# Kernel tuning notes

Hardware: AMD Instinct MI355X
Metric: run time of the kernel (lower is better)

## Reference

```python
import jax, jax.numpy as jnp
import numpy as np

B = 131072          # batch of fermion configurations
S = 256             # sys_size
NUP = 16            # num_fillings[0]
NDOWN = 16          # num_fillings[1]


def _random_occupancy(rng, b, s, nfill):
    # exactly `nfill` ones per row, uniformly random positions
    r = rng.random((b, s))
    perm_rank = np.argsort(r, axis=1).argsort(axis=1)  # a random permutation per row
    return (perm_rank < nfill).astype(np.float32)


def setup_inputs() -> dict:
    rng = np.random.default_rng(0)
    cfg_up = _random_occupancy(rng, B, S, NUP)
    cfg_down = _random_occupancy(rng, B, S, NDOWN)
    config_fermion = jnp.asarray(np.concatenate([cfg_up, cfg_down], axis=1))  # (B, 2S)
    key = jax.random.key(0)
    k1, k2 = jax.random.split(key)
    states_up = jax.random.normal(k1, (S, NUP), dtype=jnp.float32)
    states_down = jax.random.normal(k2, (S, NDOWN), dtype=jnp.float32)
    return {"config_fermion": config_fermion, "states_up": states_up, "states_down": states_down}


def reference(config_fermion, states_up, states_down):
    s = states_up.shape[0]
    nup = states_up.shape[1]
    ndown = states_down.shape[1]
    cfg_up = config_fermion[:, :s]      # (B, S) of {0,1}
    cfg_down = config_fermion[:, s:]
    # indices of occupied sites, ascending (torch.nonzero order); top_k breaks
    # ties by lowest index, then sort ascending
    idx_up = jnp.sort(jax.lax.top_k(cfg_up, nup)[1], axis=1)        # (B, Nup)
    idx_down = jnp.sort(jax.lax.top_k(cfg_down, ndown)[1], axis=1)  # (B, Ndown)
    mats_up = states_up[idx_up]         # (B, Nup, Nup) gather of orbital rows
    mats_down = states_down[idx_down]   # (B, Ndown, Ndown)
    det_up = jnp.linalg.det(mats_up)
    det_down = jnp.linalg.det(mats_down)
    return det_up * det_down
```

## Files before the change

### kernel.cpp

```cpp
#include <hip/hip_runtime.h>

static __device__ __forceinline__ unsigned umax2(unsigned a, unsigned b) { return a > b ? a : b; }

static __device__ __forceinline__ float qb(float v, int sel) {
    int i = __float_as_int(v), r;
    switch (sel) {
        case 0:  r = __builtin_amdgcn_update_dpp(0, i, 0x00, 0xF, 0xF, true); break;
        case 1:  r = __builtin_amdgcn_update_dpp(0, i, 0x55, 0xF, 0xF, true); break;
        case 2:  r = __builtin_amdgcn_update_dpp(0, i, 0xAA, 0xF, 0xF, true); break;
        default: r = __builtin_amdgcn_update_dpp(0, i, 0xFF, 0xF, 0xF, true); break;
    }
    return __int_as_float(r);
}

static __device__ __forceinline__ int mbcnt64(unsigned long long m, int acc) {
    acc = __builtin_amdgcn_mbcnt_lo((unsigned)m, acc);
    acc = __builtin_amdgcn_mbcnt_hi((unsigned)(m >> 32), acc);
    return acc;
}

__global__ __launch_bounds__(256) void slater_det_main(
    const float* __restrict__ cfg,
    const float* __restrict__ sup,
    const float* __restrict__ sdn,
    float* __restrict__ out,
    unsigned* __restrict__ ws_count,
    unsigned* __restrict__ ws_rec,
    unsigned cap)
{
    __shared__ __align__(16) int idx_lds[4][16][16];

    const int tid  = threadIdx.x;
    const int wave = tid >> 6;
    const int lane = tid & 63;
    const int wb0  = (blockIdx.x * 4 + wave) * 8;

    float4 c[16];
#pragma unroll
    for (int d = 0; d < 16; ++d) {
        const float* p = cfg + (size_t)wb0 * 512 + (size_t)d * 256 + (size_t)lane * 4;
        c[d] = *(const float4*)p;
    }
#pragma unroll
    for (int d = 0; d < 16; ++d) {
        float4 v = c[d];
        bool n0 = v.x != 0.f, n1 = v.y != 0.f, n2 = v.z != 0.f, n3 = v.w != 0.f;
        unsigned long long b0 = __ballot(n0);
        unsigned long long b1 = __ballot(n1);
        unsigned long long b2 = __ballot(n2);
        unsigned long long b3 = __ballot(n3);
        int base = mbcnt64(b3, mbcnt64(b2, mbcnt64(b1, mbcnt64(b0, 0))));
        int pos = lane * 4;
        int r = base;
        if (n0 && r < 16) idx_lds[wave][d][r] = pos;
        r += n0;
        if (n1 && r < 16) idx_lds[wave][d][r] = pos + 1;
        r += n1;
        if (n2 && r < 16) idx_lds[wave][d][r] = pos + 2;
        r += n2;
        if (n3 && r < 16) idx_lds[wave][d][r] = pos + 3;
    }
    asm volatile("s_waitcnt lgkmcnt(0)" ::: "memory");
    __builtin_amdgcn_sched_barrier(0);

    const int g = lane >> 2;
    const int q = lane & 3;
    const int4 ri = *(const int4*)&idx_lds[wave][g][q * 4];
    const float* tab = (g & 1) ? sdn : sup;
    const int rid[4] = {ri.x, ri.y, ri.z, ri.w};

    float rr[4][16];
#pragma unroll
    for (int j = 0; j < 4; ++j) {
        const float* p = tab + (size_t)rid[j] * 16;
        float4 a = *(const float4*)(p + 0);
        float4 b = *(const float4*)(p + 4);
        float4 e = *(const float4*)(p + 8);
        float4 f = *(const float4*)(p + 12);
        rr[j][0]=a.x;  rr[j][1]=a.y;  rr[j][2]=a.z;  rr[j][3]=a.w;
        rr[j][4]=b.x;  rr[j][5]=b.y;  rr[j][6]=b.z;  rr[j][7]=b.w;
        rr[j][8]=e.x;  rr[j][9]=e.y;  rr[j][10]=e.z; rr[j][11]=e.w;
        rr[j][12]=f.x; rr[j][13]=f.y; rr[j][14]=f.z; rr[j][15]=f.w;
    }

    float det = 1.f;
    bool bad = false;
#pragma unroll
    for (int k = 0; k < 16; ++k) {
        const int sel = k >> 2;
        const int jp  = k & 3;
        float piv = qb(rr[jp][k], sel);
        det *= piv;
        bad = bad || (fabsf(piv) < 1e-4f);
        float inv = __builtin_amdgcn_rcpf(piv);
        float f0 = rr[0][k] * inv;
        float f1 = rr[1][k] * inv;
        float f2 = rr[2][k] * inv;
        float f3 = rr[3][k] * inv;
#pragma unroll
        for (int cc = k + 1; cc < 16; ++cc) {
            float pcc = qb(rr[jp][cc], sel);
            rr[0][cc] = __builtin_fmaf(-f0, pcc, rr[0][cc]);
            rr[1][cc] = __builtin_fmaf(-f1, pcc, rr[1][cc]);
            rr[2][cc] = __builtin_fmaf(-f2, pcc, rr[2][cc]);
            rr[3][cc] = __builtin_fmaf(-f3, pcc, rr[3][cc]);
        }
    }

    int badflag = bad ? 1 : 0;
    int partnerbad = __shfl_xor(badflag, 4);
    if ((badflag | partnerbad) && (lane & 7) == 0) {
        unsigned slot = atomicAdd(ws_count, 1u);
        if (slot < cap) {
            unsigned* rec = ws_rec + slot * 12;
            rec[0] = (unsigned)(wb0 + (lane >> 3));
            const int gU = lane >> 2;
#pragma unroll
            for (int t = 0; t < 4; ++t) {
                const int* iu = &idx_lds[wave][gU][t * 4];
                const int* id = &idx_lds[wave][gU | 1][t * 4];
                rec[1 + t] = (unsigned)iu[0] | ((unsigned)iu[1] << 8)
                           | ((unsigned)iu[2] << 16) | ((unsigned)iu[3] << 24);
                rec[5 + t] = (unsigned)id[0] | ((unsigned)id[1] << 8)
                           | ((unsigned)id[2] << 16) | ((unsigned)id[3] << 24);
            }
        }
    }

    float prod = det * __shfl_xor(det, 4);
    if ((lane & 7) == 0) out[wb0 + (lane >> 3)] = prod;
}

__global__ __launch_bounds__(256) void slater_det_cleanup(
    const float* __restrict__ sup,
    const float* __restrict__ sdn,
    float* __restrict__ out,
    const unsigned* __restrict__ ws_count,
    const unsigned* __restrict__ ws_rec,
    unsigned cap)
{
    unsigned n = *ws_count;
    if (n > cap) n = cap;
    const int tid  = blockIdx.x * 256 + threadIdx.x;
    const int unit = tid >> 3;
    const int nunits = (int)(gridDim.x * 256) >> 3;
    const int l8   = threadIdx.x & 7;
    const int wl   = threadIdx.x & 63;
    const int q    = wl & 3;
    const int gbase = wl & ~3;

    for (unsigned item = unit; item < n; item += nunits) {
        const unsigned* rec = ws_rec + item * 12;
        const unsigned batch = rec[0];
        const int half = l8 >> 2;
        const unsigned pk = rec[1 + half * 4 + q];
        const int rid[4] = { (int)(pk & 255u), (int)((pk >> 8) & 255u),
                             (int)((pk >> 16) & 255u), (int)(pk >> 24) };
        const float* tab = half ? sdn : sup;

        float rr[4][16];
#pragma unroll
        for (int j = 0; j < 4; ++j) {
            const float* p = tab + (size_t)rid[j] * 16;
            float4 a = *(const float4*)(p + 0);
            float4 b = *(const float4*)(p + 4);
            float4 e = *(const float4*)(p + 8);
            float4 f = *(const float4*)(p + 12);
            rr[j][0]=a.x;  rr[j][1]=a.y;  rr[j][2]=a.z;  rr[j][3]=a.w;
            rr[j][4]=b.x;  rr[j][5]=b.y;  rr[j][6]=b.z;  rr[j][7]=b.w;
            rr[j][8]=e.x;  rr[j][9]=e.y;  rr[j][10]=e.z; rr[j][11]=e.w;
            rr[j][12]=f.x; rr[j][13]=f.y; rr[j][14]=f.z; rr[j][15]=f.w;
        }

        unsigned am = 0xFu;
        float fdet = 1.f;
        int flips = 0;
#pragma unroll
        for (int k = 0; k < 16; ++k) {
            unsigned a0 = (__float_as_uint(rr[0][k]) & 0x7FFFFFF0u) | (unsigned)(q*4+0);
            unsigned a1 = (__float_as_uint(rr[1][k]) & 0x7FFFFFF0u) | (unsigned)(q*4+1);
            unsigned a2 = (__float_as_uint(rr[2][k]) & 0x7FFFFFF0u) | (unsigned)(q*4+2);
            unsigned a3 = (__float_as_uint(rr[3][k]) & 0x7FFFFFF0u) | (unsigned)(q*4+3);
            unsigned key0 = (am & 1u) ? a0 : (unsigned)(q*4+0);
            unsigned key1 = (am & 2u) ? a1 : (unsigned)(q*4+1);
            unsigned key2 = (am & 4u) ? a2 : (unsigned)(q*4+2);
            unsigned key3 = (am & 8u) ? a3 : (unsigned)(q*4+3);
            unsigned kloc = umax2(umax2(key0, key1), umax2(key2, key3));
            int jloc = (int)(kloc & 3u);
            float crow[16];
#pragma unroll
            for (int cc = k; cc < 16; ++cc) {
                float t01 = (jloc & 1) ? rr[1][cc] : rr[0][cc];
                float t23 = (jloc & 1) ? rr[3][cc] : rr[2][cc];
                crow[cc] = (jloc & 2) ? t23 : t01;
            }
            unsigned ko = kloc;
            ko = umax2(ko, (unsigned)__shfl_xor((int)ko, 1));
            ko = umax2(ko, (unsigned)__shfl_xor((int)ko, 2));
            int p   = (int)(ko & 15u);
            int src = gbase | (p >> 2);
            float prow[16];
#pragma unroll
            for (int cc = k; cc < 16; ++cc) prow[cc] = __shfl(crow[cc], src);
            float piv = prow[k];
            fdet *= piv;
            int t = p - q * 4;
            unsigned mlt = (t <= 0) ? 0u : ((t >= 4) ? 0xFu : ((1u << t) - 1u));
            int cnt = __popc(am & mlt);
            cnt += __shfl_xor(cnt, 1);
            cnt += __shfl_xor(cnt, 2);
            flips += cnt;
            if (q == (p >> 2)) am &= ~(1u << (p & 3));
            float inv = 1.0f / piv;
            float f0 = rr[0][k] * inv;
            float f1 = rr[1][k] * inv;
            float f2 = rr[2][k] * inv;
            float f3 = rr[3][k] * inv;
#pragma unroll
            for (int cc = k + 1; cc < 16; ++cc) {
                rr[0][cc] = __builtin_fmaf(-f0, prow[cc], rr[0][cc]);
                rr[1][cc] = __builtin_fmaf(-f1, prow[cc], rr[1][cc]);
                rr[2][cc] = __builtin_fmaf(-f2, prow[cc], rr[2][cc]);
                rr[3][cc] = __builtin_fmaf(-f3, prow[cc], rr[3][cc]);
            }
        }
        float det = (flips & 1) ? -fdet : fdet;
        float prod = det * __shfl_xor(det, 4);
        if (l8 == 0) out[batch] = prod;
    }
}

extern "C" void kernel_launch(void* const* d_in, const int* in_sizes, int n_in,
                              void* d_out, int out_size, void* d_ws, size_t ws_size,
                              hipStream_t stream) {
    const float* cfg = (const float*)d_in[0];
    const float* sup = (const float*)d_in[1];
    const float* sdn = (const float*)d_in[2];
    float* outp = (float*)d_out;
    unsigned* ws_count = (unsigned*)d_ws;
    unsigned* ws_rec   = (unsigned*)d_ws + 4;
    unsigned cap = (unsigned)((ws_size - 16) / 48);
    const int B = in_sizes[0] / 512;
    const int blocks = B / 32;

    hipMemsetAsync(d_ws, 0, 16, stream);
    slater_det_main<<<blocks, 256, 0, stream>>>(cfg, sup, sdn, outp,
                                                ws_count, ws_rec, cap);
    slater_det_cleanup<<<16, 256, 0, stream>>>(sup, sdn, outp,
                                               ws_count, ws_rec, cap);
}
```

Baseline: 69.49 us.

## Make main kernel persistent and prefetch next chunk during elimination

The main kernel becomes a persistent grid of 1024 blocks, with each wave looping over chunks of 8 configurations in a grid-stride pattern. The first half of the next chunk's configuration rows is prefetched into registers while the current determinant elimination runs, so global loads overlap with compute. The bad-pivot check now uses a running minimum, and the r<16 guards on the index stores are dropped, which assumes exactly 16 occupied sites per half. The risks are the extra live registers from the prefetch buffer lowering occupancy, and LDS index reuse across iterations with no barrier beyond the lgkmcnt wait.

```diff
diff --git a/kernel.cpp b/kernel.cpp
--- a/kernel.cpp
+++ b/kernel.cpp
@@ -26,109 +26,146 @@
     float* __restrict__ out,
     unsigned* __restrict__ ws_count,
     unsigned* __restrict__ ws_rec,
-    unsigned cap)
+    unsigned cap,
+    int nchunks)
 {
     __shared__ __align__(16) int idx_lds[4][16][16];
 
     const int tid  = threadIdx.x;
     const int wave = tid >> 6;
     const int lane = tid & 63;
-    const int wb0  = (blockIdx.x * 4 + wave) * 8;
-
-    float4 c[16];
-#pragma unroll
-    for (int d = 0; d < 16; ++d) {
-        const float* p = cfg + (size_t)wb0 * 512 + (size_t)d * 256 + (size_t)lane * 4;
-        c[d] = *(const float4*)p;
-    }
-#pragma unroll
-    for (int d = 0; d < 16; ++d) {
-        float4 v = c[d];
-        bool n0 = v.x != 0.f, n1 = v.y != 0.f, n2 = v.z != 0.f, n3 = v.w != 0.f;
-        unsigned long long b0 = __ballot(n0);
-        unsigned long long b1 = __ballot(n1);
-        unsigned long long b2 = __ballot(n2);
-        unsigned long long b3 = __ballot(n3);
-        int base = mbcnt64(b3, mbcnt64(b2, mbcnt64(b1, mbcnt64(b0, 0))));
-        int pos = lane * 4;
-        int r = base;
-        if (n0 && r < 16) idx_lds[wave][d][r] = pos;
-        r += n0;
-        if (n1 && r < 16) idx_lds[wave][d][r] = pos + 1;
-        r += n1;
-        if (n2 && r < 16) idx_lds[wave][d][r] = pos + 2;
-        r += n2;
-        if (n3 && r < 16) idx_lds[wave][d][r] = pos + 3;
-    }
-    asm volatile("s_waitcnt lgkmcnt(0)" ::: "memory");
-    __builtin_amdgcn_sched_barrier(0);
+    const int wgid = blockIdx.x * 4 + wave;
+    const int nw   = gridDim.x * 4;
 
     const int g = lane >> 2;
     const int q = lane & 3;
-    const int4 ri = *(const int4*)&idx_lds[wave][g][q * 4];
     const float* tab = (g & 1) ? sdn : sup;
-    const int rid[4] = {ri.x, ri.y, ri.z, ri.w};
-
-    float rr[4][16];
-#pragma unroll
-    for (int j = 0; j < 4; ++j) {
-        const float* p = tab + (size_t)rid[j] * 16;
-        float4 a = *(const float4*)(p + 0);
-        float4 b = *(const float4*)(p + 4);
-        float4 e = *(const float4*)(p + 8);
-        float4 f = *(const float4*)(p + 12);
-        rr[j][0]=a.x;  rr[j][1]=a.y;  rr[j][2]=a.z;  rr[j][3]=a.w;
-        rr[j][4]=b.x;  rr[j][5]=b.y;  rr[j][6]=b.z;  rr[j][7]=b.w;
-        rr[j][8]=e.x;  rr[j][9]=e.y;  rr[j][10]=e.z; rr[j][11]=e.w;
-        rr[j][12]=f.x; rr[j][13]=f.y; rr[j][14]=f.z; rr[j][15]=f.w;
+
+    float4 c[8];
+    int cur = wgid;
+    if (cur >= nchunks) return;
+
+#pragma unroll
+    for (int d = 0; d < 8; ++d)
+        c[d] = *(const float4*)(cfg + (size_t)cur * 4096 + (size_t)d * 256 + (size_t)lane * 4);
+
+    while (cur < nchunks) {
+        const int nxt = cur + nw;
+
+#pragma unroll
+        for (int d = 0; d < 8; ++d) {
+            float4 v = c[d];
+            bool n0 = v.x != 0.f, n1 = v.y != 0.f, n2 = v.z != 0.f, n3 = v.w != 0.f;
+            unsigned long long b0 = __ballot(n0);
+            unsigned long long b1 = __ballot(n1);
+            unsigned long long b2 = __ballot(n2);
+            unsigned long long b3 = __ballot(n3);
+            int r = mbcnt64(b3, mbcnt64(b2, mbcnt64(b1, mbcnt64(b0, 0))));
+            int pos = lane * 4;
+            if (n0) idx_lds[wave][d][r] = pos;
+            r += n0;
+            if (n1) idx_lds[wave][d][r] = pos + 1;
+            r += n1;
+            if (n2) idx_lds[wave][d][r] = pos + 2;
+            r += n2;
+            if (n3) idx_lds[wave][d][r] = pos + 3;
+        }
+#pragma unroll
+        for (int d = 0; d < 8; ++d)
+            c[d] = *(const float4*)(cfg + (size_t)cur * 4096 + (size_t)(d + 8) * 256 + (size_t)lane * 4);
+#pragma unroll
+        for (int d = 0; d < 8; ++d) {
+            float4 v = c[d];
+            bool n0 = v.x != 0.f, n1 = v.y != 0.f, n2 = v.z != 0.f, n3 = v.w != 0.f;
+            unsigned long long b0 = __ballot(n0);
+            unsigned long long b1 = __ballot(n1);
+            unsigned long long b2 = __ballot(n2);
+            unsigned long long b3 = __ballot(n3);
+            int r = mbcnt64(b3, mbcnt64(b2, mbcnt64(b1, mbcnt64(b0, 0))));
+            int pos = lane * 4;
+            if (n0) idx_lds[wave][d + 8][r] = pos;
+            r += n0;
+            if (n1) idx_lds[wave][d + 8][r] = pos + 1;
+            r += n1;
+            if (n2) idx_lds[wave][d + 8][r] = pos + 2;
+            r += n2;
+            if (n3) idx_lds[wave][d + 8][r] = pos + 3;
+        }
+        asm volatile("s_waitcnt lgkmcnt(0)" ::: "memory");
+
+        const int4 ri = *(const int4*)&idx_lds[wave][g][q * 4];
+        const int rid[4] = {ri.x, ri.y, ri.z, ri.w};
+
+        float rr[4][16];
+#pragma unroll
+        for (int j = 0; j < 4; ++j) {
+            const float* p = tab + (size_t)rid[j] * 16;
+            float4 a = *(const float4*)(p + 0);
+            float4 b = *(const float4*)(p + 4);
+            float4 e = *(const float4*)(p + 8);
+            float4 f = *(const float4*)(p + 12);
+            rr[j][0]=a.x;  rr[j][1]=a.y;  rr[j][2]=a.z;  rr[j][3]=a.w;
+            rr[j][4]=b.x;  rr[j][5]=b.y;  rr[j][6]=b.z;  rr[j][7]=b.w;
+            rr[j][8]=e.x;  rr[j][9]=e.y;  rr[j][10]=e.z; rr[j][11]=e.w;
+            rr[j][12]=f.x; rr[j][13]=f.y; rr[j][14]=f.z; rr[j][15]=f.w;
+        }
+
+        if (nxt < nchunks) {
+#pragma unroll
+            for (int d = 0; d < 8; ++d)
+                c[d] = *(const float4*)(cfg + (size_t)nxt * 4096 + (size_t)d * 256 + (size_t)lane * 4);
+        }
+
+        float det = 1.f;
+        float minpiv = 1.f;
+#pragma unroll
+        for (int k = 0; k < 16; ++k) {
+            const int sel = k >> 2;
+            const int jp  = k & 3;
+            float piv = qb(rr[jp][k], sel);
+            det *= piv;
+            minpiv = fminf(minpiv, fabsf(piv));
+            float inv = __builtin_amdgcn_rcpf(piv);
+            float f0 = rr[0][k] * inv;
+            float f1 = rr[1][k] * inv;
+            float f2 = rr[2][k] * inv;
+            float f3 = rr[3][k] * inv;
+#pragma unroll
+            for (int cc = k + 1; cc < 16; ++cc) {
+                float pcc = qb(rr[jp][cc], sel);
+                rr[0][cc] = __builtin_fmaf(-f0, pcc, rr[0][cc]);
+                rr[1][cc] = __builtin_fmaf(-f1, pcc, rr[1][cc]);
+                rr[2][cc] = __builtin_fmaf(-f2, pcc, rr[2][cc]);
+                rr[3][cc] = __builtin_fmaf(-f3, pcc, rr[3][cc]);
+            }
+        }
+        bool bad = minpiv < 1e-4f;
+
+        int badflag = bad ? 1 : 0;
+        int partnerbad = __shfl_xor(badflag, 4);
+        if ((badflag | partnerbad) && (lane & 7) == 0) {
+            unsigned slot = atomicAdd(ws_count, 1u);
+            if (slot < cap) {
+                unsigned* rec = ws_rec + slot * 12;
+                rec[0] = (unsigned)(cur * 8 + (lane >> 3));
+                const int gU = lane >> 2;
+#pragma unroll
+                for (int t = 0; t < 4; ++t) {
+                    const int* iu = &idx_lds[wave][gU][t * 4];
+                    const int* id = &idx_lds[wave][gU | 1][t * 4];
+                    rec[1 + t] = (unsigned)iu[0] | ((unsigned)iu[1] << 8)
+                               | ((unsigned)iu[2] << 16) | ((unsigned)iu[3] << 24);
+                    rec[5 + t] = (unsigned)id[0] | ((unsigned)id[1] << 8)
+                               | ((unsigned)id[2] << 16) | ((unsigned)id[3] << 24);
+                }
+            }
+        }
+
+        float prod = det * __shfl_xor(det, 4);
+        if ((lane & 7) == 0) out[cur * 8 + (lane >> 3)] = prod;
+
+        cur = nxt;
     }
-
-    float det = 1.f;
-    bool bad = false;
-#pragma unroll
-    for (int k = 0; k < 16; ++k) {
-        const int sel = k >> 2;
-        const int jp  = k & 3;
-        float piv = qb(rr[jp][k], sel);
-        det *= piv;
-        bad = bad || (fabsf(piv) < 1e-4f);
-        float inv = __builtin_amdgcn_rcpf(piv);
-        float f0 = rr[0][k] * inv;
-        float f1 = rr[1][k] * inv;
-        float f2 = rr[2][k] * inv;
-        float f3 = rr[3][k] * inv;
-#pragma unroll
-        for (int cc = k + 1; cc < 16; ++cc) {
-            float pcc = qb(rr[jp][cc], sel);
-            rr[0][cc] = __builtin_fmaf(-f0, pcc, rr[0][cc]);
-            rr[1][cc] = __builtin_fmaf(-f1, pcc, rr[1][cc]);
-            rr[2][cc] = __builtin_fmaf(-f2, pcc, rr[2][cc]);
-            rr[3][cc] = __builtin_fmaf(-f3, pcc, rr[3][cc]);
-        }
-    }
-
-    int badflag = bad ? 1 : 0;
-    int partnerbad = __shfl_xor(badflag, 4);
-    if ((badflag | partnerbad) && (lane & 7) == 0) {
-        unsigned slot = atomicAdd(ws_count, 1u);
-        if (slot < cap) {
-            unsigned* rec = ws_rec + slot * 12;
-            rec[0] = (unsigned)(wb0 + (lane >> 3));
-            const int gU = lane >> 2;
-#pragma unroll
-            for (int t = 0; t < 4; ++t) {
-                const int* iu = &idx_lds[wave][gU][t * 4];
-                const int* id = &idx_lds[wave][gU | 1][t * 4];
-                rec[1 + t] = (unsigned)iu[0] | ((unsigned)iu[1] << 8)
-                           | ((unsigned)iu[2] << 16) | ((unsigned)iu[3] << 24);
-                rec[5 + t] = (unsigned)id[0] | ((unsigned)id[1] << 8)
-                           | ((unsigned)id[2] << 16) | ((unsigned)id[3] << 24);
-            }
-        }
-    }
-
-    float prod = det * __shfl_xor(det, 4);
-    if ((lane & 7) == 0) out[wb0 + (lane >> 3)] = prod;
 }
 
 __global__ __launch_bounds__(256) void slater_det_cleanup(
@@ -241,11 +278,11 @@
     unsigned* ws_rec   = (unsigned*)d_ws + 4;
     unsigned cap = (unsigned)((ws_size - 16) / 48);
     const int B = in_sizes[0] / 512;
-    const int blocks = B / 32;
+    const int nchunks = B / 8;
 
     hipMemsetAsync(d_ws, 0, 16, stream);
-    slater_det_main<<<blocks, 256, 0, stream>>>(cfg, sup, sdn, outp,
-                                                ws_count, ws_rec, cap);
+    slater_det_main<<<1024, 256, 0, stream>>>(cfg, sup, sdn, outp,
+                                              ws_count, ws_rec, cap, nchunks);
     slater_det_cleanup<<<16, 256, 0, stream>>>(sup, sdn, outp,
                                                ws_count, ws_rec, cap);
 }
```

Result: faster. 67.52 us (-2.8%).

## Add warp-specialized producer/consumer pipeline streaming configs into an LDS ring

Applied to the files above, without the earlier changes.

Rewrites the main kernel as a producer/consumer design. One wave streams configuration rows into a 16-slot LDS ring using async global_load_lds with a prefetch depth of 12. Three consumer waves spin on per-slot ready and free flags, extract occupied indices and compute the determinants. Each block now handles 128 configs instead of 32, so there are fewer blocks. The aim is to overlap the memory-bound config loads with compute, at the cost of dedicating a quarter of the waves to loading plus spin-wait synchronisation overhead and lower occupancy from the larger LDS footprint.

```diff
diff --git a/kernel.cpp b/kernel.cpp
--- a/kernel.cpp
+++ b/kernel.cpp
@@ -1,4 +1,8 @@
 #include <hip/hip_runtime.h>
+
+#define NBPB 128
+#define RS   16
+#define PD   12
 
 static __device__ __forceinline__ unsigned umax2(unsigned a, unsigned b) { return a > b ? a : b; }
 
@@ -19,7 +23,13 @@
     return acc;
 }
 
-__global__ __launch_bounds__(256) void slater_det_main(
+static __device__ __forceinline__ void gload16(const float* g, void* l) {
+    __builtin_amdgcn_global_load_lds(
+        (const __attribute__((address_space(1))) unsigned*)g,
+        (__attribute__((address_space(3))) unsigned*)l, 16, 0, 0);
+}
+
+__global__ __launch_bounds__(256) void slater_pc(
     const float* __restrict__ cfg,
     const float* __restrict__ sup,
     const float* __restrict__ sdn,
@@ -28,107 +38,139 @@
     unsigned* __restrict__ ws_rec,
     unsigned cap)
 {
-    __shared__ __align__(16) int idx_lds[4][16][16];
+    __shared__ __align__(16) unsigned char ring[RS][2048];
+    __shared__ int idx_scr[3][8][2][16];
+    __shared__ int readyf[RS];
+    __shared__ int freef[RS];
 
     const int tid  = threadIdx.x;
     const int wave = tid >> 6;
     const int lane = tid & 63;
-    const int wb0  = (blockIdx.x * 4 + wave) * 8;
-
-    float4 c[16];
-#pragma unroll
-    for (int d = 0; d < 16; ++d) {
-        const float* p = cfg + (size_t)wb0 * 512 + (size_t)d * 256 + (size_t)lane * 4;
-        c[d] = *(const float4*)p;
+    const int b0   = blockIdx.x * NBPB;
+
+    if (tid < RS) { readyf[tid] = 0; freef[tid] = 0; }
+    __syncthreads();
+
+    volatile int* vready = readyf;
+    volatile int* vfree  = freef;
+
+    if (wave == 3) {
+        for (int s = 0; s < PD; ++s) {
+            const float* g = cfg + (size_t)(b0 + s) * 512 + (size_t)lane * 4;
+            gload16(g,       &ring[s][0]);
+            gload16(g + 256, &ring[s][1024]);
+        }
+        for (int s = 0; s < NBPB; ++s) {
+            const int t = s + PD;
+            if (t < NBPB) {
+                const int k = t & (RS - 1), gen = t >> 4;
+                while (vfree[k] != gen) __builtin_amdgcn_s_sleep(2);
+                const float* g = cfg + (size_t)(b0 + t) * 512 + (size_t)lane * 4;
+                gload16(g,       &ring[k][0]);
+                gload16(g + 256, &ring[k][1024]);
+                asm volatile("s_waitcnt vmcnt(24)" ::: "memory");
+            } else {
+                asm volatile("s_waitcnt vmcnt(0)" ::: "memory");
+            }
+            if (lane == 0) vready[s & (RS - 1)] = s + 1;
+        }
+    } else {
+        const int g = lane >> 2;
+        const int q = lane & 3;
+        const float* tab = (g & 1) ? sdn : sup;
+
+        for (int grp = wave; grp < NBPB / 8; grp += 3) {
+            for (int j = 0; j < 8; ++j) {
+                const int b = grp * 8 + j, k = b & (RS - 1);
+                while (vready[k] != b + 1) __builtin_amdgcn_s_sleep(2);
+                __builtin_amdgcn_sched_barrier(0);
+#pragma unroll
+                for (int h = 0; h < 2; ++h) {
+                    float4 v = *(const float4*)&ring[k][h * 1024 + lane * 16];
+                    bool n0 = v.x != 0.f, n1 = v.y != 0.f, n2 = v.z != 0.f, n3 = v.w != 0.f;
+                    unsigned long long m0 = __ballot(n0);
+                    unsigned long long m1 = __ballot(n1);
+                    unsigned long long m2 = __ballot(n2);
+                    unsigned long long m3 = __ballot(n3);
+                    int r = mbcnt64(m3, mbcnt64(m2, mbcnt64(m1, mbcnt64(m0, 0))));
+                    int pos = lane * 4;
+                    if (n0) idx_scr[wave][j][h][r] = pos;
+                    r += n0;
+                    if (n1) idx_scr[wave][j][h][r] = pos + 1;
+                    r += n1;
+                    if (n2) idx_scr[wave][j][h][r] = pos + 2;
+                    r += n2;
+                    if (n3) idx_scr[wave][j][h][r] = pos + 3;
+                }
+                asm volatile("s_waitcnt lgkmcnt(0)" ::: "memory");
+                if (lane == 0) vfree[k] = (b >> 4) + 1;
+            }
+
+            const int4 ri = *(const int4*)&idx_scr[wave][g >> 1][g & 1][q * 4];
+            const int rid[4] = {ri.x, ri.y, ri.z, ri.w};
+            float rr[4][16];
+#pragma unroll
+            for (int j = 0; j < 4; ++j) {
+                const float* p = tab + (size_t)rid[j] * 16;
+                float4 a = *(const float4*)(p + 0);
+                float4 b = *(const float4*)(p + 4);
+                float4 e = *(const float4*)(p + 8);
+                float4 f = *(const float4*)(p + 12);
+                rr[j][0]=a.x;  rr[j][1]=a.y;  rr[j][2]=a.z;  rr[j][3]=a.w;
+                rr[j][4]=b.x;  rr[j][5]=b.y;  rr[j][6]=b.z;  rr[j][7]=b.w;
+                rr[j][8]=e.x;  rr[j][9]=e.y;  rr[j][10]=e.z; rr[j][11]=e.w;
+                rr[j][12]=f.x; rr[j][13]=f.y; rr[j][14]=f.z; rr[j][15]=f.w;
+            }
+
+            float det = 1.f;
+            float minpiv = 1.f;
+#pragma unroll
+            for (int k = 0; k < 16; ++k) {
+                const int sel = k >> 2;
+                const int jp  = k & 3;
+                float piv = qb(rr[jp][k], sel);
+                det *= piv;
+                minpiv = fminf(minpiv, fabsf(piv));
+                float inv = __builtin_amdgcn_rcpf(piv);
+                float f0 = rr[0][k] * inv;
+                float f1 = rr[1][k] * inv;
+                float f2 = rr[2][k] * inv;
+                float f3 = rr[3][k] * inv;
+#pragma unroll
+                for (int cc = k + 1; cc < 16; ++cc) {
+                    float pcc = qb(rr[jp][cc], sel);
+                    rr[0][cc] = __builtin_fmaf(-f0, pcc, rr[0][cc]);
+                    rr[1][cc] = __builtin_fmaf(-f1, pcc, rr[1][cc]);
+                    rr[2][cc] = __builtin_fmaf(-f2, pcc, rr[2][cc]);
+                    rr[3][cc] = __builtin_fmaf(-f3, pcc, rr[3][cc]);
+                }
+            }
+            bool bad = minpiv < 1e-4f;
+
+            int badflag = bad ? 1 : 0;
+            int partnerbad = __shfl_xor(badflag, 4);
+            if ((badflag | partnerbad) && (lane & 7) == 0) {
+                unsigned slot = atomicAdd(ws_count, 1u);
+                if (slot < cap) {
+                    unsigned* rec = ws_rec + slot * 12;
+                    const int j = lane >> 3;
+                    rec[0] = (unsigned)(b0 + grp * 8 + j);
+#pragma unroll
+                    for (int t = 0; t < 4; ++t) {
+                        const int* iu = &idx_scr[wave][j][0][t * 4];
+                        const int* id = &idx_scr[wave][j][1][t * 4];
+                        rec[1 + t] = (unsigned)iu[0] | ((unsigned)iu[1] << 8)
+                                   | ((unsigned)iu[2] << 16) | ((unsigned)iu[3] << 24);
+                        rec[5 + t] = (unsigned)id[0] | ((unsigned)id[1] << 8)
+                                   | ((unsigned)id[2] << 16) | ((unsigned)id[3] << 24);
+                    }
+                }
+            }
+
+            float prod = det * __shfl_xor(det, 4);
+            if ((lane & 7) == 0) out[b0 + grp * 8 + (lane >> 3)] = prod;
+        }
     }
-#pragma unroll
-    for (int d = 0; d < 16; ++d) {
-        float4 v = c[d];
-        bool n0 = v.x != 0.f, n1 = v.y != 0.f, n2 = v.z != 0.f, n3 = v.w != 0.f;
-        unsigned long long b0 = __ballot(n0);
-        unsigned long long b1 = __ballot(n1);
-        unsigned long long b2 = __ballot(n2);
-        unsigned long long b3 = __ballot(n3);
-        int base = mbcnt64(b3, mbcnt64(b2, mbcnt64(b1, mbcnt64(b0, 0))));
-        int pos = lane * 4;
-        int r = base;
-        if (n0 && r < 16) idx_lds[wave][d][r] = pos;
-        r += n0;
-        if (n1 && r < 16) idx_lds[wave][d][r] = pos + 1;
-        r += n1;
-        if (n2 && r < 16) idx_lds[wave][d][r] = pos + 2;
-        r += n2;
-        if (n3 && r < 16) idx_lds[wave][d][r] = pos + 3;
-    }
-    asm volatile("s_waitcnt lgkmcnt(0)" ::: "memory");
-    __builtin_amdgcn_sched_barrier(0);
-
-    const int g = lane >> 2;
-    const int q = lane & 3;
-    const int4 ri = *(const int4*)&idx_lds[wave][g][q * 4];
-    const float* tab = (g & 1) ? sdn : sup;
-    const int rid[4] = {ri.x, ri.y, ri.z, ri.w};
-
-    float rr[4][16];
-#pragma unroll
-    for (int j = 0; j < 4; ++j) {
-        const float* p = tab + (size_t)rid[j] * 16;
-        float4 a = *(const float4*)(p + 0);
-        float4 b = *(const float4*)(p + 4);
-        float4 e = *(const float4*)(p + 8);
-        float4 f = *(const float4*)(p + 12);
-        rr[j][0]=a.x;  rr[j][1]=a.y;  rr[j][2]=a.z;  rr[j][3]=a.w;
-        rr[j][4]=b.x;  rr[j][5]=b.y;  rr[j][6]=b.z;  rr[j][7]=b.w;
-        rr[j][8]=e.x;  rr[j][9]=e.y;  rr[j][10]=e.z; rr[j][11]=e.w;
-        rr[j][12]=f.x; rr[j][13]=f.y; rr[j][14]=f.z; rr[j][15]=f.w;
-    }
-
-    float det = 1.f;
-    bool bad = false;
-#pragma unroll
-    for (int k = 0; k < 16; ++k) {
-        const int sel = k >> 2;
-        const int jp  = k & 3;
-        float piv = qb(rr[jp][k], sel);
-        det *= piv;
-        bad = bad || (fabsf(piv) < 1e-4f);
-        float inv = __builtin_amdgcn_rcpf(piv);
-        float f0 = rr[0][k] * inv;
-        float f1 = rr[1][k] * inv;
-        float f2 = rr[2][k] * inv;
-        float f3 = rr[3][k] * inv;
-#pragma unroll
-        for (int cc = k + 1; cc < 16; ++cc) {
-            float pcc = qb(rr[jp][cc], sel);
-            rr[0][cc] = __builtin_fmaf(-f0, pcc, rr[0][cc]);
-            rr[1][cc] = __builtin_fmaf(-f1, pcc, rr[1][cc]);
-            rr[2][cc] = __builtin_fmaf(-f2, pcc, rr[2][cc]);
-            rr[3][cc] = __builtin_fmaf(-f3, pcc, rr[3][cc]);
-        }
-    }
-
-    int badflag = bad ? 1 : 0;
-    int partnerbad = __shfl_xor(badflag, 4);
-    if ((badflag | partnerbad) && (lane & 7) == 0) {
-        unsigned slot = atomicAdd(ws_count, 1u);
-        if (slot < cap) {
-            unsigned* rec = ws_rec + slot * 12;
-            rec[0] = (unsigned)(wb0 + (lane >> 3));
-            const int gU = lane >> 2;
-#pragma unroll
-            for (int t = 0; t < 4; ++t) {
-                const int* iu = &idx_lds[wave][gU][t * 4];
-                const int* id = &idx_lds[wave][gU | 1][t * 4];
-                rec[1 + t] = (unsigned)iu[0] | ((unsigned)iu[1] << 8)
-                           | ((unsigned)iu[2] << 16) | ((unsigned)iu[3] << 24);
-                rec[5 + t] = (unsigned)id[0] | ((unsigned)id[1] << 8)
-                           | ((unsigned)id[2] << 16) | ((unsigned)id[3] << 24);
-            }
-        }
-    }
-
-    float prod = det * __shfl_xor(det, 4);
-    if ((lane & 7) == 0) out[wb0 + (lane >> 3)] = prod;
 }
 
 __global__ __launch_bounds__(256) void slater_det_cleanup(
@@ -241,11 +283,11 @@
     unsigned* ws_rec   = (unsigned*)d_ws + 4;
     unsigned cap = (unsigned)((ws_size - 16) / 48);
     const int B = in_sizes[0] / 512;
-    const int blocks = B / 32;
+    const int blocks = B / NBPB;
 
     hipMemsetAsync(d_ws, 0, 16, stream);
-    slater_det_main<<<blocks, 256, 0, stream>>>(cfg, sup, sdn, outp,
-                                                ws_count, ws_rec, cap);
+    slater_pc<<<blocks, 256, 0, stream>>>(cfg, sup, sdn, outp,
+                                          ws_count, ws_rec, cap);
     slater_det_cleanup<<<16, 256, 0, stream>>>(sup, sdn, outp,
                                                ws_count, ws_rec, cap);
 }
```

Measured after the change: 115.2 us. 1.66x slower.
